# Kernel optimization log

Hardware: AMD Instinct MI355X
Metric: run time of the kernel (lower is better)

Reference implementation:

```python
import jax, jax.numpy as jnp
import numpy as np

N_HEAD, D_MODEL, D_K, D_V = 16, 1024, 64, 64
B, S = 4, 2048


def setup_inputs() -> dict:
    key = jax.random.key(0)
    ks = jax.random.split(key, 11)
    s = 0.02
    return {
        "q": jax.random.normal(ks[0], (B, S, D_MODEL), jnp.float32),
        "k": jax.random.normal(ks[1], (B, S, D_MODEL), jnp.float32),
        "v": jax.random.normal(ks[2], (B, S, D_MODEL), jnp.float32),
        "Wq": jax.random.normal(ks[3], (D_MODEL, N_HEAD * D_K), jnp.float32) * s,
        "bq": jnp.zeros((N_HEAD * D_K,), jnp.float32),
        "Wk": jax.random.normal(ks[4], (D_MODEL, N_HEAD * D_K), jnp.float32) * s,
        "bk": jnp.zeros((N_HEAD * D_K,), jnp.float32),
        "Wv": jax.random.normal(ks[5], (D_MODEL, N_HEAD * D_V), jnp.float32) * s,
        "bv": jnp.zeros((N_HEAD * D_V,), jnp.float32),
        "Wo": jax.random.normal(ks[6], (N_HEAD * D_V, D_MODEL), jnp.float32) * s,
        "bo": jnp.zeros((D_MODEL,), jnp.float32),
    }


def reference(q, k, v, Wq, bq, Wk, bk, Wv, bv, Wo, bo):
    b, s, _ = q.shape
    # project and split heads: [B,S,H,Dk] -> [B,H,S,Dk]
    qh = (q @ Wq + bq).reshape(b, s, N_HEAD, D_K).transpose(0, 2, 1, 3)
    kh = (k @ Wk + bk).reshape(b, s, N_HEAD, D_K).transpose(0, 2, 1, 3)
    vh = (v @ Wv + bv).reshape(b, s, N_HEAD, D_V).transpose(0, 2, 1, 3)
    scale = 1.0 / jnp.sqrt(jnp.float32(D_K))
    scores = jnp.einsum("bhqd,bhkd->bhqk", qh, kh) * scale  # [B,H,S,S]
    atten = jax.nn.softmax(scores, axis=-1)
    out = jnp.einsum("bhqk,bhkd->bhqd", atten, vh)  # [B,H,S,Dv]
    out = out.transpose(0, 2, 1, 3).reshape(b, s, N_HEAD * D_V)
    return out @ Wo + bo
```

## Files before the change

kernel.cpp:

```cpp
#include <hip/hip_runtime.h>

typedef unsigned short u16;
typedef __attribute__((ext_vector_type(4))) float f32x4;
typedef __attribute__((ext_vector_type(16))) float f32x16;
typedef __attribute__((ext_vector_type(8))) short bf16x8;
typedef __attribute__((ext_vector_type(4))) u16 u16x4;
typedef __attribute__((ext_vector_type(8))) u16 u16x8;

#define MFMA16(a, b, c) __builtin_amdgcn_mfma_f32_16x16x32_bf16((a), (b), (c), 0, 0, 0)
#define MFMA32(a, b, c) __builtin_amdgcn_mfma_f32_32x32x16_bf16((a), (b), (c), 0, 0, 0)

__device__ __forceinline__ u16 f2bf(float f) {
  union { float f; unsigned u; } x; x.f = f;
  unsigned r = x.u + 0x7fffu + ((x.u >> 16) & 1u);
  return (u16)(r >> 16);
}

__device__ __forceinline__ unsigned cvtpk(float lo, float hi) {
  unsigned r;
  asm("v_cvt_pk_bf16_f32 %0, %1, %2" : "=v"(r) : "v"(lo), "v"(hi));
  return r;
}

__device__ __forceinline__ void gl_lds16(const void* g, void* l) {
  __builtin_amdgcn_global_load_lds((const __attribute__((address_space(1))) void*)g,
                                   (__attribute__((address_space(3))) void*)l,
                                   16, 0, 0);
}

__global__ __launch_bounds__(256) void cvtT_k(const float* __restrict__ W0, const float* __restrict__ W1,
                                              const float* __restrict__ W2, const float* __restrict__ W3,
                                              u16* __restrict__ T0, u16* __restrict__ T1,
                                              u16* __restrict__ T2, u16* __restrict__ T3) {
  __shared__ u16 t[64][72];
  const float* W; u16* T;
  switch (blockIdx.z) {
    case 0: W = W0; T = T0; break;
    case 1: W = W1; T = T1; break;
    case 2: W = W2; T = T2; break;
    default: W = W3; T = T3; break;
  }
  const int tid = threadIdx.x;
  const int tr = blockIdx.x, tc = blockIdx.y;
#pragma unroll
  for (int i = 0; i < 4; ++i) {
    int row = i * 16 + (tid >> 4);
    int c4 = tid & 15;
    float4 v = *(const float4*)&W[(size_t)(tr * 64 + row) * 1024 + tc * 64 + c4 * 4];
    t[row][c4 * 4 + 0] = f2bf(v.x);
    t[row][c4 * 4 + 1] = f2bf(v.y);
    t[row][c4 * 4 + 2] = f2bf(v.z);
    t[row][c4 * 4 + 3] = f2bf(v.w);
  }
  __syncthreads();
#pragma unroll
  for (int i = 0; i < 4; ++i) {
    int orow = i * 16 + (tid >> 4);
    int occ = tid & 15;
    u16x4 o;
#pragma unroll
    for (int j = 0; j < 4; ++j) o[j] = t[occ * 4 + j][orow];
    *(u16x4*)&T[(size_t)(tc * 64 + orow) * 1024 + tr * 64 + occ * 4] = o;
  }
}

__global__ __launch_bounds__(512) void gemm_qkv_k(const float* __restrict__ Xq, const float* __restrict__ Xk,
                                                  const float* __restrict__ Xv, const u16* __restrict__ WTb,
                                                  const float* __restrict__ bq, const float* __restrict__ bk,
                                                  const float* __restrict__ bv,
                                                  u16* __restrict__ Qh, u16* __restrict__ Kh,
                                                  u16* __restrict__ Vt, float qscale) {
  __shared__ u16 As[2][128 * 64];
  __shared__ u16 Bs[2][128 * 64];
  const int tid = threadIdx.x;
  const int lane = tid & 63;
  const int w = tid >> 6;
  const int which = blockIdx.y >> 3;
  const int m0 = blockIdx.x * 128;
  const int n0 = (blockIdx.y & 7) * 128;
  const float* X = which == 0 ? Xq : (which == 1 ? Xk : Xv);
  const u16* WT = WTb + (size_t)which * 1024 * 1024;
  const float* bias = which == 0 ? bq : (which == 1 ? bk : bv);
  const int wr = (w >> 2) * 64;
  const int wc = (w & 3) * 32;
  const int srow = lane >> 3;
  const int sch = (lane & 7) * 8;
  const int arow = tid >> 3;
  const int acol = (tid & 7) * 8;
  f32x4 acc[4][2] = {};
  float4 va[4];

#define BSTAGE(slot_, ks_) do {                                                             \
    int k0_ = (ks_) * 64;                                                                   \
    gl_lds16(WT + (size_t)(n0 + w * 16 + srow) * 1024 + k0_ + sch, &Bs[slot_][(w * 16) * 64]);     \
    gl_lds16(WT + (size_t)(n0 + w * 16 + 8 + srow) * 1024 + k0_ + sch, &Bs[slot_][(w * 16 + 8) * 64]); \
  } while (0)

#define ALOAD(ks_) do {                                                                     \
    int k0_ = (ks_) * 64;                                                                   \
    va[0] = *(const float4*)&X[(size_t)(m0 + arow) * 1024 + k0_ + acol];                    \
    va[1] = *(const float4*)&X[(size_t)(m0 + arow) * 1024 + k0_ + acol + 4];                \
    va[2] = *(const float4*)&X[(size_t)(m0 + 64 + arow) * 1024 + k0_ + acol];               \
    va[3] = *(const float4*)&X[(size_t)(m0 + 64 + arow) * 1024 + k0_ + acol + 4];           \
  } while (0)

  BSTAGE(0, 0);
  ALOAD(0);

  for (int ks = 0; ks < 16; ++ks) {
#pragma unroll
    for (int i = 0; i < 2; ++i) {
      int row = i * 64 + arow;
      const float4 vlo = va[2 * i], vhi = va[2 * i + 1];
      u16x8 o;
      o[0] = f2bf(vlo.x); o[1] = f2bf(vlo.y); o[2] = f2bf(vlo.z); o[3] = f2bf(vlo.w);
      o[4] = f2bf(vhi.x); o[5] = f2bf(vhi.y); o[6] = f2bf(vhi.z); o[7] = f2bf(vhi.w);
      *(u16x8*)&As[ks & 1][row * 64 + acol] = o;
    }
    asm volatile("s_waitcnt lgkmcnt(0)" ::: "memory");
    __builtin_amdgcn_s_barrier();
    if (ks < 15) { BSTAGE((ks + 1) & 1, ks + 1); ALOAD(ks + 1); }
    __builtin_amdgcn_sched_barrier(0);

    const u16* Ac = As[ks & 1];
    const u16* Bc = Bs[ks & 1];
#pragma unroll
    for (int kk = 0; kk < 2; ++kk) {
      bf16x8 a[4], b[2];
#pragma unroll
      for (int t = 0; t < 4; ++t)
        a[t] = *(const bf16x8*)&Ac[(wr + t * 16 + (lane & 15)) * 64 + kk * 32 + (lane >> 4) * 8];
#pragma unroll
      for (int u = 0; u < 2; ++u)
        b[u] = *(const bf16x8*)&Bc[(wc + u * 16 + (lane & 15)) * 64 + kk * 32 + (lane >> 4) * 8];
#pragma unroll
      for (int mi = 0; mi < 4; ++mi)
#pragma unroll
        for (int ni = 0; ni < 2; ++ni)
          acc[mi][ni] = MFMA16(a[mi], b[ni], acc[mi][ni]);
    }
  }
#undef BSTAGE
#undef ALOAD

  const int lr = (lane >> 4) * 4;
  const int lc = lane & 15;
  if (which <= 1) {
    u16* ob = which == 0 ? Qh : Kh;
    float scale = which == 0 ? qscale : 1.0f;
#pragma unroll
    for (int mi = 0; mi < 4; ++mi)
#pragma unroll
      for (int ni = 0; ni < 2; ++ni) {
        int n = n0 + wc + ni * 16 + lc;
        float bb = bias[n];
        int h = n >> 6, d = n & 63;
#pragma unroll
        for (int r = 0; r < 4; ++r) {
          int m = m0 + wr + mi * 16 + lr + r;
          int b = m >> 11, s = m & 2047;
          ob[(((size_t)(b * 16 + h) * 2048 + s) << 6) + d] = f2bf((acc[mi][ni][r] + bb) * scale);
        }
      }
  } else {
#pragma unroll
    for (int mi = 0; mi < 4; ++mi)
#pragma unroll
      for (int ni = 0; ni < 2; ++ni) {
        int n = n0 + wc + ni * 16 + lc;
        float bb = bias[n];
        int h = n >> 6, d = n & 63;
        int m = m0 + wr + mi * 16 + lr;
        int b = m >> 11, s = m & 2047;
        u16x4 pk;
#pragma unroll
        for (int r = 0; r < 4; ++r) pk[r] = f2bf(acc[mi][ni][r] + bb);
        *(u16x4*)&Vt[((size_t)(b * 16 + h) * 64 + d) * 2048 + s] = pk;
      }
  }
}

__global__ __launch_bounds__(256) void gemm_o_k(const u16* __restrict__ X, const u16* __restrict__ WT,
                                                const float* __restrict__ bias, float* __restrict__ out) {
  __shared__ u16 As[128 * 64];
  __shared__ u16 Bs[128 * 64];
  const int tid = threadIdx.x;
  const int lane = tid & 63;
  const int w = tid >> 6;
  const int m0 = blockIdx.x * 128;
  const int n0 = blockIdx.y * 128;
  const int wr = (w >> 1) * 64;
  const int wc = (w & 1) * 64;
  const int srow = lane >> 3;
  const int sch = (lane & 7) * 8;
  f32x4 acc[4][4] = {};

  for (int ks = 0; ks < 16; ++ks) {
    const int k0 = ks * 64;
#pragma unroll
    for (int i = 0; i < 4; ++i) {
      int row = i * 32 + w * 8 + srow;
      gl_lds16(X + (size_t)(m0 + row) * 1024 + k0 + sch, &As[(i * 32 + w * 8) * 64]);
      gl_lds16(WT + (size_t)(n0 + row) * 1024 + k0 + sch, &Bs[(i * 32 + w * 8) * 64]);
    }
    __syncthreads();
#pragma unroll
    for (int kk = 0; kk < 2; ++kk) {
      bf16x8 a[4], b[4];
#pragma unroll
      for (int t = 0; t < 4; ++t) {
        a[t] = *(const bf16x8*)&As[(wr + t * 16 + (lane & 15)) * 64 + kk * 32 + (lane >> 4) * 8];
        b[t] = *(const bf16x8*)&Bs[(wc + t * 16 + (lane & 15)) * 64 + kk * 32 + (lane >> 4) * 8];
      }
#pragma unroll
      for (int mi = 0; mi < 4; ++mi)
#pragma unroll
        for (int ni = 0; ni < 4; ++ni)
          acc[mi][ni] = MFMA16(a[mi], b[ni], acc[mi][ni]);
    }
    __syncthreads();
  }

  const int lr = (lane >> 4) * 4;
  const int lc = lane & 15;
#pragma unroll
  for (int mi = 0; mi < 4; ++mi)
#pragma unroll
    for (int ni = 0; ni < 4; ++ni) {
      int n = n0 + wc + ni * 16 + lc;
      float bb = bias[n];
#pragma unroll
      for (int r = 0; r < 4; ++r) {
        int m = m0 + wr + mi * 16 + lr + r;
        out[(size_t)m * 1024 + n] = acc[mi][ni][r] + bb;
      }
    }
}

__global__ __launch_bounds__(512) void attn_k(const u16* __restrict__ Qh, const u16* __restrict__ Kh,
                                              const u16* __restrict__ Vt, u16* __restrict__ AO) {
  __shared__ u16 SMEM[4 * 8192];
  const int lane = threadIdx.x & 63, w = threadIdx.x >> 6;
  const int hi = lane >> 5, q = lane & 31;

  const int id = blockIdx.x;
  const int bh = ((id >> 3) & 7) * 8 + (id & 7);
  const int qt = id >> 6;
  const int q0 = qt * 256 + w * 32;

  const u16* Qb = Qh + (size_t)bh * 2048 * 64;
  const u16* Kb = Kh + (size_t)bh * 2048 * 64;
  const u16* Vb = Vt + (size_t)bh * 64 * 2048;

  bf16x8 qf[4];
#pragma unroll
  for (int c = 0; c < 4; ++c)
    qf[c] = *(const bf16x8*)&Qb[(size_t)(q0 + q) * 64 + c * 16 + hi * 8];

  bf16x8 onesf;
#pragma unroll
  for (int i = 0; i < 8; ++i) onesf[i] = (short)0x3F80;

  f32x16 o0 = {}, o1 = {}, ol = {};
  const int lo8 = lane * 8;

  const int srowK = (w & 1) * 32 + q;
  const int sck = ((w >> 1) * 2 + hi) * 8;

#define STAGE(slot_, kt_) do {                                                       \
    int k0_ = (kt_) * 64;                                                            \
    gl_lds16(Kb + (size_t)(k0_ + srowK) * 64 + sck, &SMEM[(slot_) * 8192 + w * 512]);          \
    gl_lds16(Vb + (size_t)srowK * 2048 + k0_ + sck, &SMEM[(slot_) * 8192 + 4096 + w * 512]);   \
  } while (0)

  STAGE(0, 0);
  STAGE(1, 1);
  STAGE(2, 2);

  for (int kt = 0; kt < 32; ++kt) {
    if (kt < 30)       asm volatile("s_waitcnt vmcnt(4)" ::: "memory");
    else if (kt == 30) asm volatile("s_waitcnt vmcnt(2)" ::: "memory");
    else               asm volatile("s_waitcnt vmcnt(0)" ::: "memory");
    __builtin_amdgcn_s_barrier();
    if (kt <= 28) STAGE((kt + 3) & 3, kt + 3);
    __builtin_amdgcn_sched_barrier(0);

    const u16* Kc = &SMEM[(kt & 3) * 8192];
    const u16* Vc = Kc + 4096;

    f32x16 s0 = {}, s1 = {};
    __builtin_amdgcn_s_setprio(1);
#pragma unroll
    for (int c = 0; c < 4; ++c) {
      bf16x8 k0 = *(const bf16x8*)&Kc[(c * 2) * 512 + lo8];
      bf16x8 k1 = *(const bf16x8*)&Kc[(c * 2 + 1) * 512 + lo8];
      s0 = MFMA32(k0, qf[c], s0);
      s1 = MFMA32(k1, qf[c], s1);
    }
    __builtin_amdgcn_s_setprio(0);

#pragma unroll
    for (int i = 0; i < 16; ++i) {
      s0[i] = __builtin_exp2f(s0[i]);
      s1[i] = __builtin_exp2f(s1[i]);
    }

    __builtin_amdgcn_s_setprio(1);
#pragma unroll
    for (int t = 0; t < 4; ++t) {
      unsigned wA, wB, wC, wD;
      if (t == 0) { wA = cvtpk(s0[0], s0[1]); wB = cvtpk(s0[2], s0[3]); wC = cvtpk(s0[4], s0[5]); wD = cvtpk(s0[6], s0[7]); }
      else if (t == 1) { wA = cvtpk(s0[8], s0[9]); wB = cvtpk(s0[10], s0[11]); wC = cvtpk(s0[12], s0[13]); wD = cvtpk(s0[14], s0[15]); }
      else if (t == 2) { wA = cvtpk(s1[0], s1[1]); wB = cvtpk(s1[2], s1[3]); wC = cvtpk(s1[4], s1[5]); wD = cvtpk(s1[6], s1[7]); }
      else { wA = cvtpk(s1[8], s1[9]); wB = cvtpk(s1[10], s1[11]); wC = cvtpk(s1[12], s1[13]); wD = cvtpk(s1[14], s1[15]); }
      asm("v_permlane32_swap_b32 %0, %1" : "+v"(wA), "+v"(wC));
      asm("v_permlane32_swap_b32 %0, %1" : "+v"(wB), "+v"(wD));
      union { unsigned u[4]; bf16x8 v; } pf;
      pf.u[0] = wA; pf.u[1] = wB; pf.u[2] = wC; pf.u[3] = wD;
      bf16x8 v0 = *(const bf16x8*)&Vc[(t * 2) * 512 + lo8];
      bf16x8 v1 = *(const bf16x8*)&Vc[(t * 2 + 1) * 512 + lo8];
      o0 = MFMA32(v0, pf.v, o0);
      o1 = MFMA32(v1, pf.v, o1);
      ol = MFMA32(onesf, pf.v, ol);
    }
    __builtin_amdgcn_s_setprio(0);
  }
#undef STAGE

  __builtin_amdgcn_s_barrier();

  float inv = 1.0f / ol[0];
  u16* ep = SMEM + w * 2048;
#pragma unroll
  for (int g = 0; g < 2; ++g) {
    const f32x16 oo = g ? o1 : o0;
#pragma unroll
    for (int j = 0; j < 8; ++j) {
      int d = g * 32 + (j & 1) * 2 + ((j >> 1) & 1) * 8 + (j >> 2) * 16 + 4 * hi;
      unsigned pw = cvtpk(oo[2 * j] * inv, oo[2 * j + 1] * inv);
      *(unsigned*)&ep[q * 64 + ((d >> 3) ^ (q & 7)) * 8 + (d & 7)] = pw;
    }
  }
  asm volatile("s_waitcnt lgkmcnt(0)" ::: "memory");
  const int b = bh >> 4, h = bh & 15;
#pragma unroll
  for (int i = 0; i < 4; ++i) {
    int r = i * 8 + (lane >> 3), c = lane & 7;
    u16x8 vv = *(const u16x8*)&ep[r * 64 + ((c ^ (r & 7)) * 8)];
    size_t row = (size_t)b * 2048 + q0 + r;
    *(u16x8*)&AO[row * 1024 + h * 64 + c * 8] = vv;
  }
}

extern "C" void kernel_launch(void* const* d_in, const int* in_sizes, int n_in,
                              void* d_out, int out_size, void* d_ws, size_t ws_size,
                              hipStream_t stream) {
  const float* q  = (const float*)d_in[0];
  const float* k  = (const float*)d_in[1];
  const float* v  = (const float*)d_in[2];
  const float* Wq = (const float*)d_in[3];
  const float* bq = (const float*)d_in[4];
  const float* Wk = (const float*)d_in[5];
  const float* bk = (const float*)d_in[6];
  const float* Wv = (const float*)d_in[7];
  const float* bv = (const float*)d_in[8];
  const float* Wo = (const float*)d_in[9];
  const float* bo = (const float*)d_in[10];
  float* out = (float*)d_out;

  char* ws = (char*)d_ws;
  const size_t SZX = (size_t)8192 * 1024 * 2;
  const size_t SZW = (size_t)1024 * 1024 * 2;
  u16* AO  = (u16*)(ws);
  u16* WTq = (u16*)(ws + 3 * SZX);
  u16* WTk = (u16*)(ws + 3 * SZX + SZW);
  u16* WTv = (u16*)(ws + 3 * SZX + 2 * SZW);
  u16* WTo = (u16*)(ws + 3 * SZX + 3 * SZW);
  u16* Qh  = (u16*)(ws + 3 * SZX + 4 * SZW);
  u16* Kh  = (u16*)(ws + 4 * SZX + 4 * SZW);
  u16* Vt  = (u16*)(ws + 5 * SZX + 4 * SZW);

  cvtT_k<<<dim3(16, 16, 4), dim3(256), 0, stream>>>(Wq, Wk, Wv, Wo, WTq, WTk, WTv, WTo);

  gemm_qkv_k<<<dim3(64, 24), dim3(512), 0, stream>>>(q, k, v, WTq, bq, bk, bv, Qh, Kh, Vt,
                                                     0.125f * 1.4426950408889634f);

  attn_k<<<dim3(512), dim3(512), 0, stream>>>(Qh, Kh, Vt, AO);

  gemm_o_k<<<dim3(64, 8), dim3(256), 0, stream>>>(AO, WTo, bo, out);
}
```

Baseline: 221.3 us.

## Store GEMM LDS tiles in MFMA-fragment order to remove bank conflicts

Rearranges the shared-memory tiles of the QKV and output-projection GEMMs so each 16-row by 32-k MFMA fragment sits in a contiguous 512-element block, ordered lane by lane. Global loads are remapped to fill this layout directly, so each wave's LDS read becomes one contiguous 16-byte-per-lane access. The old row-major 64-wide layout caused LDS bank conflicts on the fragment reads. The trade-off is less coalesced global loads, since each lane now reads 16 bytes from a different row with only four lanes sharing a row segment.

```diff
diff --git a/kernel.cpp b/kernel.cpp
--- a/kernel.cpp
+++ b/kernel.cpp
@@ -70,8 +70,8 @@
                                                   const float* __restrict__ bv,
                                                   u16* __restrict__ Qh, u16* __restrict__ Kh,
                                                   u16* __restrict__ Vt, float qscale) {
-  __shared__ u16 As[2][128 * 64];
-  __shared__ u16 Bs[2][128 * 64];
+  __shared__ u16 As[2][16 * 512];
+  __shared__ u16 Bs[2][16 * 512];
   const int tid = threadIdx.x;
   const int lane = tid & 63;
   const int w = tid >> 6;
@@ -83,25 +83,27 @@
   const float* bias = which == 0 ? bq : (which == 1 ? bk : bv);
   const int wr = (w >> 2) * 64;
   const int wc = (w & 3) * 32;
-  const int srow = lane >> 3;
-  const int sch = (lane & 7) * 8;
-  const int arow = tid >> 3;
-  const int acol = (tid & 7) * 8;
+  const int l15 = lane & 15, l4 = lane >> 4;
+  const int lo8 = lane * 8;
   f32x4 acc[4][2] = {};
   float4 va[4];
 
-#define BSTAGE(slot_, ks_) do {                                                             \
-    int k0_ = (ks_) * 64;                                                                   \
-    gl_lds16(WT + (size_t)(n0 + w * 16 + srow) * 1024 + k0_ + sch, &Bs[slot_][(w * 16) * 64]);     \
-    gl_lds16(WT + (size_t)(n0 + w * 16 + 8 + srow) * 1024 + k0_ + sch, &Bs[slot_][(w * 16 + 8) * 64]); \
+  const size_t aRow = (size_t)(m0 + w * 16 + l15) * 1024;
+  const size_t bRow = (size_t)(n0 + w * 16 + l15) * 1024;
+  const int kOff = l4 * 8;
+
+#define BSTAGE(slot_, ks_) do {                                                   \
+    int k0_ = (ks_) * 64;                                                         \
+    gl_lds16(WT + bRow + k0_ + kOff,      &Bs[slot_][(w * 2 + 0) * 512]);         \
+    gl_lds16(WT + bRow + k0_ + 32 + kOff, &Bs[slot_][(w * 2 + 1) * 512]);         \
   } while (0)
 
-#define ALOAD(ks_) do {                                                                     \
-    int k0_ = (ks_) * 64;                                                                   \
-    va[0] = *(const float4*)&X[(size_t)(m0 + arow) * 1024 + k0_ + acol];                    \
-    va[1] = *(const float4*)&X[(size_t)(m0 + arow) * 1024 + k0_ + acol + 4];                \
-    va[2] = *(const float4*)&X[(size_t)(m0 + 64 + arow) * 1024 + k0_ + acol];               \
-    va[3] = *(const float4*)&X[(size_t)(m0 + 64 + arow) * 1024 + k0_ + acol + 4];           \
+#define ALOAD(ks_) do {                                                           \
+    int k0_ = (ks_) * 64;                                                         \
+    va[0] = *(const float4*)&X[aRow + k0_ + kOff];                                \
+    va[1] = *(const float4*)&X[aRow + k0_ + kOff + 4];                            \
+    va[2] = *(const float4*)&X[aRow + k0_ + 32 + kOff];                           \
+    va[3] = *(const float4*)&X[aRow + k0_ + 32 + kOff + 4];                       \
   } while (0)
 
   BSTAGE(0, 0);
@@ -109,13 +111,12 @@
 
   for (int ks = 0; ks < 16; ++ks) {
 #pragma unroll
-    for (int i = 0; i < 2; ++i) {
-      int row = i * 64 + arow;
-      const float4 vlo = va[2 * i], vhi = va[2 * i + 1];
+    for (int kk = 0; kk < 2; ++kk) {
+      const float4 vlo = va[2 * kk], vhi = va[2 * kk + 1];
       u16x8 o;
       o[0] = f2bf(vlo.x); o[1] = f2bf(vlo.y); o[2] = f2bf(vlo.z); o[3] = f2bf(vlo.w);
       o[4] = f2bf(vhi.x); o[5] = f2bf(vhi.y); o[6] = f2bf(vhi.z); o[7] = f2bf(vhi.w);
-      *(u16x8*)&As[ks & 1][row * 64 + acol] = o;
+      *(u16x8*)&As[ks & 1][(w * 2 + kk) * 512 + lo8] = o;
     }
     asm volatile("s_waitcnt lgkmcnt(0)" ::: "memory");
     __builtin_amdgcn_s_barrier();
@@ -129,10 +130,10 @@
       bf16x8 a[4], b[2];
 #pragma unroll
       for (int t = 0; t < 4; ++t)
-        a[t] = *(const bf16x8*)&Ac[(wr + t * 16 + (lane & 15)) * 64 + kk * 32 + (lane >> 4) * 8];
+        a[t] = *(const bf16x8*)&Ac[(((w >> 2) * 4 + t) * 2 + kk) * 512 + lo8];
 #pragma unroll
       for (int u = 0; u < 2; ++u)
-        b[u] = *(const bf16x8*)&Bc[(wc + u * 16 + (lane & 15)) * 64 + kk * 32 + (lane >> 4) * 8];
+        b[u] = *(const bf16x8*)&Bc[(((w & 3) * 2 + u) * 2 + kk) * 512 + lo8];
 #pragma unroll
       for (int mi = 0; mi < 4; ++mi)
 #pragma unroll
@@ -182,8 +183,8 @@
 
 __global__ __launch_bounds__(256) void gemm_o_k(const u16* __restrict__ X, const u16* __restrict__ WT,
                                                 const float* __restrict__ bias, float* __restrict__ out) {
-  __shared__ u16 As[128 * 64];
-  __shared__ u16 Bs[128 * 64];
+  __shared__ u16 As[16 * 512];
+  __shared__ u16 Bs[16 * 512];
   const int tid = threadIdx.x;
   const int lane = tid & 63;
   const int w = tid >> 6;
@@ -191,17 +192,22 @@
   const int n0 = blockIdx.y * 128;
   const int wr = (w >> 1) * 64;
   const int wc = (w & 1) * 64;
-  const int srow = lane >> 3;
-  const int sch = (lane & 7) * 8;
+  const int l15 = lane & 15, l4 = lane >> 4;
+  const int lo8 = lane * 8;
+  const int kOff = l4 * 8;
   f32x4 acc[4][4] = {};
 
   for (int ks = 0; ks < 16; ++ks) {
     const int k0 = ks * 64;
 #pragma unroll
-    for (int i = 0; i < 4; ++i) {
-      int row = i * 32 + w * 8 + srow;
-      gl_lds16(X + (size_t)(m0 + row) * 1024 + k0 + sch, &As[(i * 32 + w * 8) * 64]);
-      gl_lds16(WT + (size_t)(n0 + row) * 1024 + k0 + sch, &Bs[(i * 32 + w * 8) * 64]);
+    for (int j = 0; j < 2; ++j) {
+      int rg = 2 * w + j;
+      const size_t ar = (size_t)(m0 + rg * 16 + l15) * 1024;
+      const size_t br = (size_t)(n0 + rg * 16 + l15) * 1024;
+      gl_lds16(X + ar + k0 + kOff,       &As[(rg * 2 + 0) * 512]);
+      gl_lds16(X + ar + k0 + 32 + kOff,  &As[(rg * 2 + 1) * 512]);
+      gl_lds16(WT + br + k0 + kOff,      &Bs[(rg * 2 + 0) * 512]);
+      gl_lds16(WT + br + k0 + 32 + kOff, &Bs[(rg * 2 + 1) * 512]);
     }
     __syncthreads();
 #pragma unroll
@@ -209,8 +215,8 @@
       bf16x8 a[4], b[4];
 #pragma unroll
       for (int t = 0; t < 4; ++t) {
-        a[t] = *(const bf16x8*)&As[(wr + t * 16 + (lane & 15)) * 64 + kk * 32 + (lane >> 4) * 8];
-        b[t] = *(const bf16x8*)&Bs[(wc + t * 16 + (lane & 15)) * 64 + kk * 32 + (lane >> 4) * 8];
+        a[t] = *(const bf16x8*)&As[(((wr >> 4) + t) * 2 + kk) * 512 + lo8];
+        b[t] = *(const bf16x8*)&Bs[(((wc >> 4) + t) * 2 + kk) * 512 + lo8];
       }
 #pragma unroll
       for (int mi = 0; mi < 4; ++mi)
```

Result: slower. 270.3 us (+22.1%).

## XOR-swizzle LDS tiles in QKV and output GEMMs, deepen A-operand prefetch

Applied to the files above, without the earlier changes.

Applies an XOR swizzle to the 16-byte chunk index of the LDS tiles in both the QKV projection and the output projection GEMMs, so the MFMA fragment reads avoid LDS bank conflicts. In the QKV kernel, the fp32 activation loads are double-buffered in registers (two register sets) and issued two k-steps ahead. They are waited on with vmcnt(4) instead of a full drain. This is meant to hide global latency better, at the cost of more registers and an unrolled body.

```diff
diff --git a/kernel.cpp b/kernel.cpp
--- a/kernel.cpp
+++ b/kernel.cpp
@@ -83,65 +83,90 @@
   const float* bias = which == 0 ? bq : (which == 1 ? bk : bv);
   const int wr = (w >> 2) * 64;
   const int wc = (w & 3) * 32;
-  const int srow = lane >> 3;
-  const int sch = (lane & 7) * 8;
+  const int l15 = lane & 15, l4 = lane >> 4, l7 = lane & 7;
+  const int sr = lane >> 3;
+  const int sc8 = ((lane & 7) ^ sr) * 8;
   const int arow = tid >> 3;
-  const int acol = (tid & 7) * 8;
+  const int ac = tid & 7;
+  const int aswz = (ac ^ (arow & 7)) * 8;
   f32x4 acc[4][2] = {};
-  float4 va[4];
-
-#define BSTAGE(slot_, ks_) do {                                                             \
-    int k0_ = (ks_) * 64;                                                                   \
-    gl_lds16(WT + (size_t)(n0 + w * 16 + srow) * 1024 + k0_ + sch, &Bs[slot_][(w * 16) * 64]);     \
-    gl_lds16(WT + (size_t)(n0 + w * 16 + 8 + srow) * 1024 + k0_ + sch, &Bs[slot_][(w * 16 + 8) * 64]); \
-  } while (0)
-
-#define ALOAD(ks_) do {                                                                     \
-    int k0_ = (ks_) * 64;                                                                   \
-    va[0] = *(const float4*)&X[(size_t)(m0 + arow) * 1024 + k0_ + acol];                    \
-    va[1] = *(const float4*)&X[(size_t)(m0 + arow) * 1024 + k0_ + acol + 4];                \
-    va[2] = *(const float4*)&X[(size_t)(m0 + 64 + arow) * 1024 + k0_ + acol];               \
-    va[3] = *(const float4*)&X[(size_t)(m0 + 64 + arow) * 1024 + k0_ + acol + 4];           \
+  float4 va_a[4], va_b[4];
+
+#define BSTAGE(slot_, ks_) do {                                                              \
+    int k0_ = (ks_) * 64;                                                                    \
+    gl_lds16(WT + (size_t)(n0 + w * 16 + sr) * 1024 + k0_ + sc8, &Bs[slot_][(w * 16) * 64]);       \
+    gl_lds16(WT + (size_t)(n0 + w * 16 + 8 + sr) * 1024 + k0_ + sc8, &Bs[slot_][(w * 16 + 8) * 64]); \
+  } while (0)
+
+#define ALOAD(VA, ks_) do {                                                                  \
+    int k0_ = (ks_) * 64;                                                                    \
+    VA[0] = *(const float4*)&X[(size_t)(m0 + arow) * 1024 + k0_ + ac * 8];                   \
+    VA[1] = *(const float4*)&X[(size_t)(m0 + arow) * 1024 + k0_ + ac * 8 + 4];               \
+    VA[2] = *(const float4*)&X[(size_t)(m0 + 64 + arow) * 1024 + k0_ + ac * 8];              \
+    VA[3] = *(const float4*)&X[(size_t)(m0 + 64 + arow) * 1024 + k0_ + ac * 8 + 4];          \
+  } while (0)
+
+#define AWRITE(VA, slot_) do {                                                               \
+    _Pragma("unroll")                                                                        \
+    for (int i_ = 0; i_ < 2; ++i_) {                                                         \
+      int row_ = i_ * 64 + arow;                                                             \
+      const float4 vlo = VA[2 * i_], vhi = VA[2 * i_ + 1];                                   \
+      u16x8 o_;                                                                              \
+      o_[0] = f2bf(vlo.x); o_[1] = f2bf(vlo.y); o_[2] = f2bf(vlo.z); o_[3] = f2bf(vlo.w);    \
+      o_[4] = f2bf(vhi.x); o_[5] = f2bf(vhi.y); o_[6] = f2bf(vhi.z); o_[7] = f2bf(vhi.w);    \
+      *(u16x8*)&As[slot_][row_ * 64 + aswz] = o_;                                            \
+    }                                                                                        \
+  } while (0)
+
+#define COMPUTE(slot_) do {                                                                  \
+    const u16* Ac_ = As[slot_];                                                              \
+    const u16* Bc_ = Bs[slot_];                                                              \
+    _Pragma("unroll")                                                                        \
+    for (int kk = 0; kk < 2; ++kk) {                                                         \
+      int cs_ = ((kk * 4 + l4) ^ l7) * 8;                                                    \
+      bf16x8 a_[4], b_[2];                                                                   \
+      _Pragma("unroll")                                                                      \
+      for (int t = 0; t < 4; ++t)                                                            \
+        a_[t] = *(const bf16x8*)&Ac_[(wr + t * 16 + l15) * 64 + cs_];                        \
+      _Pragma("unroll")                                                                      \
+      for (int u = 0; u < 2; ++u)                                                            \
+        b_[u] = *(const bf16x8*)&Bc_[(wc + u * 16 + l15) * 64 + cs_];                        \
+      _Pragma("unroll")                                                                      \
+      for (int mi = 0; mi < 4; ++mi)                                                         \
+        _Pragma("unroll")                                                                    \
+        for (int ni = 0; ni < 2; ++ni)                                                       \
+          acc[mi][ni] = MFMA16(a_[mi], b_[ni], acc[mi][ni]);                                 \
+    }                                                                                        \
+  } while (0)
+
+#define BODY(ks_, VA, DO_B, DO_A, VM4) do {                                                  \
+    AWRITE(VA, (ks_) & 1);                                                                   \
+    asm volatile("s_waitcnt lgkmcnt(0)" ::: "memory");                                       \
+    if (VM4) asm volatile("s_waitcnt vmcnt(4)" ::: "memory");                                \
+    else     asm volatile("s_waitcnt vmcnt(0)" ::: "memory");                                \
+    __builtin_amdgcn_s_barrier();                                                            \
+    if (DO_B) BSTAGE(((ks_) + 1) & 1, (ks_) + 1);                                            \
+    if (DO_A) ALOAD(VA, (ks_) + 2);                                                          \
+    __builtin_amdgcn_sched_barrier(0);                                                       \
+    COMPUTE((ks_) & 1);                                                                      \
   } while (0)
 
   BSTAGE(0, 0);
-  ALOAD(0);
-
-  for (int ks = 0; ks < 16; ++ks) {
-#pragma unroll
-    for (int i = 0; i < 2; ++i) {
-      int row = i * 64 + arow;
-      const float4 vlo = va[2 * i], vhi = va[2 * i + 1];
-      u16x8 o;
-      o[0] = f2bf(vlo.x); o[1] = f2bf(vlo.y); o[2] = f2bf(vlo.z); o[3] = f2bf(vlo.w);
-      o[4] = f2bf(vhi.x); o[5] = f2bf(vhi.y); o[6] = f2bf(vhi.z); o[7] = f2bf(vhi.w);
-      *(u16x8*)&As[ks & 1][row * 64 + acol] = o;
-    }
-    asm volatile("s_waitcnt lgkmcnt(0)" ::: "memory");
-    __builtin_amdgcn_s_barrier();
-    if (ks < 15) { BSTAGE((ks + 1) & 1, ks + 1); ALOAD(ks + 1); }
-    __builtin_amdgcn_sched_barrier(0);
-
-    const u16* Ac = As[ks & 1];
-    const u16* Bc = Bs[ks & 1];
-#pragma unroll
-    for (int kk = 0; kk < 2; ++kk) {
-      bf16x8 a[4], b[2];
-#pragma unroll
-      for (int t = 0; t < 4; ++t)
-        a[t] = *(const bf16x8*)&Ac[(wr + t * 16 + (lane & 15)) * 64 + kk * 32 + (lane >> 4) * 8];
-#pragma unroll
-      for (int u = 0; u < 2; ++u)
-        b[u] = *(const bf16x8*)&Bc[(wc + u * 16 + (lane & 15)) * 64 + kk * 32 + (lane >> 4) * 8];
-#pragma unroll
-      for (int mi = 0; mi < 4; ++mi)
-#pragma unroll
-        for (int ni = 0; ni < 2; ++ni)
-          acc[mi][ni] = MFMA16(a[mi], b[ni], acc[mi][ni]);
-    }
-  }
+  ALOAD(va_a, 0);
+  ALOAD(va_b, 1);
+
+  for (int i = 0; i < 7; ++i) {
+    BODY(2 * i, va_a, 1, 1, 1);
+    BODY(2 * i + 1, va_b, 1, 1, 1);
+  }
+  BODY(14, va_a, 1, 0, 1);
+  BODY(15, va_b, 0, 0, 0);
+
 #undef BSTAGE
 #undef ALOAD
+#undef AWRITE
+#undef COMPUTE
+#undef BODY
 
   const int lr = (lane >> 4) * 4;
   const int lc = lane & 15;
@@ -191,26 +216,28 @@
   const int n0 = blockIdx.y * 128;
   const int wr = (w >> 1) * 64;
   const int wc = (w & 1) * 64;
-  const int srow = lane >> 3;
-  const int sch = (lane & 7) * 8;
+  const int l15 = lane & 15, l4 = lane >> 4, l7 = lane & 7;
+  const int sr = lane >> 3;
+  const int sc8 = ((lane & 7) ^ sr) * 8;
   f32x4 acc[4][4] = {};
 
   for (int ks = 0; ks < 16; ++ks) {
     const int k0 = ks * 64;
 #pragma unroll
-    for (int i = 0; i < 4; ++i) {
-      int row = i * 32 + w * 8 + srow;
-      gl_lds16(X + (size_t)(m0 + row) * 1024 + k0 + sch, &As[(i * 32 + w * 8) * 64]);
-      gl_lds16(WT + (size_t)(n0 + row) * 1024 + k0 + sch, &Bs[(i * 32 + w * 8) * 64]);
+    for (int j = 0; j < 4; ++j) {
+      int rb = w * 32 + j * 8;
+      gl_lds16(X + (size_t)(m0 + rb + sr) * 1024 + k0 + sc8, &As[rb * 64]);
+      gl_lds16(WT + (size_t)(n0 + rb + sr) * 1024 + k0 + sc8, &Bs[rb * 64]);
     }
     __syncthreads();
 #pragma unroll
     for (int kk = 0; kk < 2; ++kk) {
+      int cs = ((kk * 4 + l4) ^ l7) * 8;
       bf16x8 a[4], b[4];
 #pragma unroll
       for (int t = 0; t < 4; ++t) {
-        a[t] = *(const bf16x8*)&As[(wr + t * 16 + (lane & 15)) * 64 + kk * 32 + (lane >> 4) * 8];
-        b[t] = *(const bf16x8*)&Bs[(wc + t * 16 + (lane & 15)) * 64 + kk * 32 + (lane >> 4) * 8];
+        a[t] = *(const bf16x8*)&As[(wr + t * 16 + l15) * 64 + cs];
+        b[t] = *(const bf16x8*)&Bs[(wc + t * 16 + l15) * 64 + cs];
       }
 #pragma unroll
       for (int mi = 0; mi < 4; ++mi)
```

Result: faster. 196.7 us (-11.1%).
